# Performance work log

Hardware: AMD Instinct MI355X
Metric: run time of the kernel (lower is better)

The kernel has to match this reference:

```python
import jax, jax.numpy as jnp
from jax import lax
import numpy as np

B = 128   # per-stream batch (hard-coded via torch.zeros(128, ...))
T = 224   # timesteps
L = 224   # per-timestep signal length
H = 12    # LSTM hidden size


def _conv_chain(x, w1, b1, w2, b2):
    # x: [N, 1, 224] -> [N, 1, 28]
    # Conv1d(k=8, s=4, p=2) -> ReLU -> MaxPool1d(k=4, s=2, p=1) -> ReLU -> Conv1d(k=3, s=1, p=1) -> ReLU
    y = lax.conv_general_dilated(x, w1, (4,), [(2, 2)]) + b1[None, :, None]          # [N,1,56]
    y = jax.nn.relu(y)
    y = lax.reduce_window(y, -jnp.inf, lax.max, (1, 1, 4), (1, 1, 2),
                          [(0, 0), (0, 0), (1, 1)])                                   # [N,1,28]
    y = jax.nn.relu(y)
    y = lax.conv_general_dilated(y, w2, (1,), [(1, 1)]) + b2[None, :, None]          # [N,1,28]
    return jax.nn.relu(y)


def _lstm_bidir(x, Wih, Whh, b):
    # x: [B, T, D]; Wih: [2, 4H, D]; Whh: [2, 4H, H]; b: [2, 4H]; gates in PyTorch order i,f,g,o
    Bn, hid = x.shape[0], Whh.shape[-1]

    def run(xs, wih, whh, bb):
        def step(carry, xt):
            h, c = carry
            g = xt @ wih.T + h @ whh.T + bb
            i, f, gg, o = jnp.split(g, 4, axis=-1)
            c = jax.nn.sigmoid(f) * c + jax.nn.sigmoid(i) * jnp.tanh(gg)
            h = jax.nn.sigmoid(o) * jnp.tanh(c)
            return (h, c), h
        h0 = jnp.zeros((Bn, hid), x.dtype)
        _, ys = lax.scan(step, (h0, h0), xs)
        return ys

    xs = jnp.swapaxes(x, 0, 1)                     # [T, B, D]
    fwd = run(xs, Wih[0], Whh[0], b[0])
    bwd = run(xs[::-1], Whh_fix := Wih[1], Whh[1], b[1])[::-1]
    return jnp.swapaxes(jnp.concatenate([fwd, bwd], axis=-1), 0, 1)  # [B, T, 2H]


def _forward(x, c1w1, c1b1, c1w2, c1b2, c2w1, c2b1, c2w2, c2b2,
             l1_0_Wih, l1_0_Whh, l1_0_b, l1_1_Wih, l1_1_Whh, l1_1_b,
             l2_0_Wih, l2_0_Whh, l2_0_b, l2_1_Wih, l2_1_Whh, l2_1_b,
             fcw1, fcb1, fcw2, fcb2, fcw3, fcb3, w1, w2):
    x1 = x[:B, 0]          # [B, 224, 224]
    x2 = x[B:2 * B, 0]     # [B, 224, 224]
    # Fuse the 224-step Python loop: fold time into the batch of the 1D conv.
    y1 = _conv_chain(x1.reshape(B * T, 1, L), c1w1, c1b1, c1w2, c1b2).reshape(B, T, 28)
    y2 = _conv_chain(x2.reshape(B * T, 1, L), c2w1, c2b1, c2w2, c2b2).reshape(B, T, 28)
    o1 = _lstm_bidir(_lstm_bidir(y1, l1_0_Wih, l1_0_Whh, l1_0_b), l1_1_Wih, l1_1_Whh, l1_1_b)
    o2 = _lstm_bidir(_lstm_bidir(y2, l2_0_Wih, l2_0_Whh, l2_0_b), l2_1_Wih, l2_1_Whh, l2_1_b)
    out = w1 * o1 + w2 * o2                       # [B, T, 24]
    out = out.reshape(B, T * 2 * H)               # [B, 5376]
    out = out @ fcw1.T + fcb1                     # [B, 1024]
    out = out @ fcw2.T + fcb2                     # [B, 192]
    return out @ fcw3.T + fcb3                    # [B, 9]


def setup_inputs():
    key = jax.random.key(0)
    ks = iter(jax.random.split(key, 48))

    def rn(shape, scale=0.1):
        return (scale * jax.random.normal(next(ks), shape)).astype(jnp.float32)

    inp = {"x": rn((2 * B, 1, T, L), 1.0)}
    for s in ("c1", "c2"):
        inp[s + "w1"] = rn((1, 1, 8))
        inp[s + "b1"] = rn((1,))
        inp[s + "w2"] = rn((1, 1, 3))
        inp[s + "b2"] = rn((1,))
    for s in ("l1", "l2"):
        for layer, din in ((0, 28), (1, 2 * H)):
            inp[f"{s}_{layer}_Wih"] = rn((2, 4 * H, din))
            inp[f"{s}_{layer}_Whh"] = rn((2, 4 * H, H))
            inp[f"{s}_{layer}_b"] = rn((2, 4 * H))
    inp["fcw1"] = rn((1024, T * 2 * H), 0.02)
    inp["fcb1"] = rn((1024,))
    inp["fcw2"] = rn((192, 1024), 0.05)
    inp["fcb2"] = rn((192,))
    inp["fcw3"] = rn((9, 192), 0.05)
    inp["fcb3"] = rn((9,))
    inp["w1"] = jnp.ones((1,), jnp.float32)
    inp["w2"] = jnp.ones((1,), jnp.float32)
    return inp


def reference(x, c1w1, c1b1, c1w2, c1b2, c2w1, c2b1, c2w2, c2b2,
              l1_0_Wih, l1_0_Whh, l1_0_b, l1_1_Wih, l1_1_Whh, l1_1_b,
              l2_0_Wih, l2_0_Whh, l2_0_b, l2_1_Wih, l2_1_Whh, l2_1_b,
              fcw1, fcb1, fcw2, fcb2, fcw3, fcb3, w1, w2):
    return _forward(x, c1w1, c1b1, c1w2, c1b2, c2w1, c2b1, c2w2, c2b2,
                    l1_0_Wih, l1_0_Whh, l1_0_b, l1_1_Wih, l1_1_Whh, l1_1_b,
                    l2_0_Wih, l2_0_Whh, l2_0_b, l2_1_Wih, l2_1_Whh, l2_1_b,
                    fcw1, fcb1, fcw2, fcb2, fcw3, fcb3, w1, w2)
```

## Files before the change

kernel.cpp:

```cpp
#include <hip/hip_runtime.h>

#define BB 128
#define TT 224
#define LL 224

typedef float v2f __attribute__((ext_vector_type(2)));

__device__ __forceinline__ float rcpf(float x){ return __builtin_amdgcn_rcpf(x); }

#if __has_builtin(__builtin_amdgcn_exp2f)
#define EXP2(x) __builtin_amdgcn_exp2f(x)
#else
#define EXP2(x) __expf((x)*0.6931471805599453f)
#endif

template<int N>
__device__ __forceinline__ float rorN(float x){
  int xi = __builtin_bit_cast(int, x);
  xi = __builtin_amdgcn_update_dpp(xi, xi, 0x120 + N, 0xf, 0xf, false);
  return __builtin_bit_cast(float, xi);
}

__device__ __forceinline__ void swap32(float& a, float& b){
  asm volatile("s_nop 1\n\tv_permlane32_swap_b32 %0, %1\n\ts_nop 1"
               : "+v"(a), "+v"(b));
}

#define LSTM_STEP(P, SS) { \
  float x1=rorN<1>(hv), x2=rorN<2>(hv), x3=rorN<3>(hv), x4=rorN<4>(hv), \
        x5=rorN<5>(hv), x6=rorN<6>(hv), x7=rorN<7>(hv), x8=rorN<8>(hv), \
        x9=rorN<9>(hv), x10=rorN<10>(hv), x11=rorN<11>(hv), x12=rorN<12>(hv), \
        x13=rorN<13>(hv), x14=rorN<14>(hv), x15=rorN<15>(hv); \
  v2f a0 = (P); \
  a0 += w[0]*(v2f){hv,hv};   a0 += w[1]*(v2f){x1,x1};   a0 += w[2]*(v2f){x2,x2};   a0 += w[3]*(v2f){x3,x3}; \
  v2f a1 = w[4]*(v2f){x4,x4};   a1 += w[5]*(v2f){x5,x5};   a1 += w[6]*(v2f){x6,x6};   a1 += w[7]*(v2f){x7,x7}; \
  v2f a2 = w[8]*(v2f){x8,x8};   a2 += w[9]*(v2f){x9,x9};   a2 += w[10]*(v2f){x10,x10}; a2 += w[11]*(v2f){x11,x11}; \
  v2f a3 = w[12]*(v2f){x12,x12}; a3 += w[13]*(v2f){x13,x13}; a3 += w[14]*(v2f){x14,x14}; a3 += w[15]*(v2f){x15,x15}; \
  v2f gg = (a0+a1)+(a2+a3); \
  v2f m  = gg*kmul; \
  v2f e  = { EXP2(m.x), EXP2(m.y) }; \
  e += (v2f){1.f,1.f}; \
  v2f d  = { rcpf(e.x), rcpf(e.y) }; \
  v2f res = ca*d + cb; \
  float p0 = res.x, p1 = res.x; swap32(p0, p1); \
  float q0 = res.y, q1 = res.y; swap32(q0, q1); \
  cst = fmaf(q0, cst, p0*p1); \
  float et = EXP2(cst*2.885390082f); \
  float dt = rcpf(et+1.f); \
  hv = q1*fmaf(-2.f, dt, 1.f); \
  hbuf[SS] = hv; }

#define FLUSH8 { \
  if (doSt){ \
    _Pragma("unroll") \
    for (int q=0;q<8;q++) outP[q*ostep] = hbuf[q]; \
  } \
  outP += 8*ostep; }

#define LSTM_PREP(WHH) \
  v2f w[16]; \
  _Pragma("unroll") \
  for (int rr=0; rr<16; rr++){ \
    int j = (u - rr) & 15; \
    bool vld = (j < 12) && (u < 12); \
    int uw = (u < 12) ? u : 0; \
    int jw = (j < 12) ? j : 0; \
    float wa = (WHH)[((rbit?24:0)  + uw)*12 + jw]; \
    float wb = (WHH)[((rbit?36:12) + uw)*12 + jw]; \
    w[rr] = (v2f){ vld ? wa : 0.f, vld ? wb : 0.f }; \
  } \
  const v2f kmul = rbit ? (v2f){2.885390082f, -1.442695041f} \
                        : (v2f){-1.442695041f, -1.442695041f}; \
  const v2f ca   = rbit ? (v2f){-2.f, 1.f} : (v2f){1.f, 1.f}; \
  const v2f cb   = rbit ? (v2f){ 1.f, 0.f} : (v2f){0.f, 0.f};

#define LSTM_CONSUME_LDS(LPRE, OUTBUF) { \
  float* preR = (LPRE) + bh*(224*48) + keff*4 + rbit*2; \
  const int sstep = dir ? -48 : 48; \
  int scb = dir ? 223*48 : 0; \
  volatile int* pv = prog; \
  while (pv[1] < 2 || pv[2] < 2) __builtin_amdgcn_s_sleep(2); \
  asm volatile("" ::: "memory"); \
  v2f pcur[8], pnext[8]; \
  _Pragma("unroll") \
  for (int i=0;i<8;i++) pcur[i]  = *(const v2f*)(preR + scb +  i   *sstep); \
  _Pragma("unroll") \
  for (int i=0;i<8;i++) pnext[i] = *(const v2f*)(preR + scb + (i+8)*sstep); \
  int lb = scb + 16*sstep; \
  float hv = 0.f, cst = 0.f; \
  float hbuf[8]; \
  const int ostep = dir ? -24 : 24; \
  float* outP = (OUTBUF) + (size_t)br*(BB*TT*24) + (size_t)b*TT*24 + dir*12 + u \
              + (size_t)(dir ? 223 : 0)*24; \
  const bool doSt = (rbit==0) && (u < 12); \
  for (int c=0;c<14;c++){ \
    LSTM_STEP(pcur[0],0) LSTM_STEP(pcur[1],1) LSTM_STEP(pcur[2],2) LSTM_STEP(pcur[3],3) \
    LSTM_STEP(pcur[4],4) LSTM_STEP(pcur[5],5) LSTM_STEP(pcur[6],6) LSTM_STEP(pcur[7],7) \
    FLUSH8 \
    if (c < 13){ \
      int nd_ = 2*c+3; \
      while (pv[1] < nd_ || pv[2] < nd_) __builtin_amdgcn_s_sleep(2); \
      asm volatile("" ::: "memory"); \
      _Pragma("unroll") \
      for (int i=0;i<8;i++) pcur[i] = *(const v2f*)(preR + lb + i*sstep); \
      lb += 8*sstep; \
    } \
    LSTM_STEP(pnext[0],0) LSTM_STEP(pnext[1],1) LSTM_STEP(pnext[2],2) LSTM_STEP(pnext[3],3) \
    LSTM_STEP(pnext[4],4) LSTM_STEP(pnext[5],5) LSTM_STEP(pnext[6],6) LSTM_STEP(pnext[7],7) \
    FLUSH8 \
    if (c < 13){ \
      int nd_ = 2*c+4; \
      while (pv[1] < nd_ || pv[2] < nd_) __builtin_amdgcn_s_sleep(2); \
      asm volatile("" ::: "memory"); \
      _Pragma("unroll") \
      for (int i=0;i<8;i++) pnext[i] = *(const v2f*)(preR + lb + i*sstep); \
      lb += 8*sstep; \
    } \
  } }

__global__ __launch_bounds__(256) void fcA_kernel(
    const float* __restrict__ fcw1, const float* __restrict__ fcw2,
    const float* __restrict__ fcw3, const float* __restrict__ fcb1,
    float* __restrict__ wpart, float* __restrict__ BCpart)
{
  __shared__ float sb[2880];
  int gb  = blockIdx.x;
  int tid = threadIdx.x;
  int s     = gb / 21;
  int jtile = gb % 21;
  float* wtp = sb;
  float* wt  = sb + 2304;
  {
    int wave = tid >> 6, lane = tid & 63;
    float acc[9];
    #pragma unroll
    for (int q=0;q<9;q++) acc[q]=0.f;
    const float* f2 = fcw2 + s*64 + lane;
    int p0 = wave*48;
    #pragma unroll 4
    for (int pp=0; pp<48; pp++){
      int p = p0 + pp;
      float v = f2[(size_t)p*1024];
      #pragma unroll
      for (int q=0;q<9;q++) acc[q] += fcw3[q*192+p]*v;
    }
    #pragma unroll
    for (int q=0;q<9;q++) wtp[wave*576 + q*64 + lane] = acc[q];
  }
  __syncthreads();
  for (int i = tid; i < 576; i += 256)
    wt[i] = wtp[i] + wtp[576+i] + wtp[1152+i] + wtp[1728+i];
  __syncthreads();

  int j = jtile*256 + tid;
  int nbase = s*64;
  float acc[9];
  #pragma unroll
  for (int o=0;o<9;o++) acc[o]=0.f;
  #pragma unroll 4
  for (int n4=0;n4<16;n4++){
    int nb = nbase + n4*4;
    float4 v4;
    v4.x = fcw1[(size_t)(nb  )*5376 + j];
    v4.y = fcw1[(size_t)(nb+1)*5376 + j];
    v4.z = fcw1[(size_t)(nb+2)*5376 + j];
    v4.w = fcw1[(size_t)(nb+3)*5376 + j];
    #pragma unroll
    for (int o=0;o<9;o++){
      float4 w4 = *(const float4*)&wt[o*64 + n4*4];
      acc[o] += v4.x*w4.x + v4.y*w4.y + v4.z*w4.z + v4.w*w4.w;
    }
  }
  #pragma unroll
  for (int o=0;o<9;o++) wpart[((size_t)s*9+o)*5376 + j] = acc[o];
  if (jtile == 0 && tid < 9){
    float bcp = 0.f;
    for (int n=0;n<64;n++) bcp += wt[tid*64+n]*fcb1[nbase+n];
    BCpart[s*9+tid] = bcp;
  }
}

__global__ __launch_bounds__(256) __attribute__((amdgpu_waves_per_eu(1,1)))
void lstm1_fused_kernel(const float* __restrict__ x,
    const float* __restrict__ whhA, const float* __restrict__ whhB,
    const float* __restrict__ wihA, const float* __restrict__ biasA,
    const float* __restrict__ wihB, const float* __restrict__ biasB,
    const float* __restrict__ c1w1, const float* __restrict__ c1b1,
    const float* __restrict__ c1w2, const float* __restrict__ c1b2,
    const float* __restrict__ c2w1, const float* __restrict__ c2b1,
    const float* __restrict__ c2w2, const float* __restrict__ c2b2,
    float* __restrict__ out)
{
  __shared__ float lpre[2*224*48];
  __shared__ float ybuf[2*224*28];
  __shared__ float c1s[16*57];
  __shared__ int prog[8];
  int tid  = threadIdx.x;
  int blk  = blockIdx.x;
  int r    = blk >> 6;
  int br   = r >> 1, dir = r & 1;
  int b0   = (blk & 63)*2;

  if (tid < 8) ((volatile int*)prog)[tid] = 0;
  __syncthreads();

  if (tid >= 64 && tid < 128){
    int p    = tid - 64;
    int rowq = p >> 2;
    int q    = p & 3;
    int bb   = rowq >> 3;
    int ti   = rowq & 7;
    int cjs  = q*14;
    const float* w1 = br ? c2w1 : c1w1;
    const float* w2 = br ? c2w2 : c1w2;
    float b1  = br ? c2b1[0] : c1b1[0];
    float b2v = br ? c2b2[0] : c1b2[0];
    float w1r[8];
    #pragma unroll
    for (int kk=0;kk<8;kk++) w1r[kk]=w1[kk];
    float w2r[3];
    #pragma unroll
    for (int kk=0;kk<3;kk++) w2r[kk]=w2[kk];
    const float* xb = x + ((size_t)(br*128 + b0 + bb))*50176;
    volatile int* pv = prog;
    int a0 = 4*cjs - 4;

    for (int g=0; g<28; ++g){
      int step = g*8 + ti;
      int t = dir ? 223-step : step;
      const float* xrow = xb + (size_t)t*224;
      float xr[64];
      #pragma unroll
      for (int qq=0; qq<16; qq++){
        int idx = a0 + 4*qq;
        if (idx >= 0 && idx <= 220){
          float4 v = *(const float4*)(xrow + idx);
          xr[4*qq]=v.x; xr[4*qq+1]=v.y; xr[4*qq+2]=v.z; xr[4*qq+3]=v.w;
        } else {
          #pragma unroll
          for (int e=0;e<4;e++){
            int ii = idx+e;
            xr[4*qq+e] = (ii>=0 && ii<224) ? xrow[ii] : 0.f;
          }
        }
      }
      #pragma unroll
      for (int e=0;e<14;e++){
        float s = b1;
        #pragma unroll
        for (int kk=0;kk<8;kk++) s += xr[4*e+2+kk]*w1r[kk];
        c1s[rowq*57 + cjs + e] = fmaxf(s, 0.f);
      }
      asm volatile("s_waitcnt lgkmcnt(0)" ::: "memory");
      const float* cr = &c1s[rowq*57];
      #pragma unroll
      for (int jj=0;jj<7;jj++){
        int j = q*7 + jj;
        float o = b2v;
        #pragma unroll
        for (int pi=0;pi<3;pi++){
          int pp = j - 1 + pi;
          float pool = 0.f;
          if (pp>=0 && pp<28){
            int i0 = 2*pp - 1;
            float m = -1e30f;
            #pragma unroll
            for (int q2=0;q2<4;q2++){
              int ii = i0+q2;
              if (ii>=0 && ii<56) m = fmaxf(m, cr[ii]);
            }
            pool = fmaxf(m, 0.f);
          }
          o += pool * w2r[pi];
        }
        ybuf[(bb*224 + t)*28 + j] = fmaxf(o, 0.f);
      }
      asm volatile("s_waitcnt lgkmcnt(0)" ::: "memory");
      if (p == 0) pv[0] = g+1;
    }
    return;
  }

  if (tid >= 128){
    int p2 = tid - 128;
    if (p2 >= 96) return;
    int fidx = (tid >> 6) - 1;
    int bb   = p2 / 48;
    int gate = p2 % 48;
    const float* wih2 = (br ? wihB : wihA) + (dir*48 + gate)*28;
    float4 wq[7];
    #pragma unroll
    for (int q=0;q<7;q++) wq[q] = ((const float4*)wih2)[q];
    float bias = (br ? biasB : biasA)[dir*48 + gate];
    int unit = gate % 12, gg = gate / 12;
    float* lrow = lpre + bb*(224*48) + unit*4 + gg;
    volatile int* pv = prog;

    for (int g=0; g<28; ++g){
      while (pv[0] < g+1) __builtin_amdgcn_s_sleep(2);
      asm volatile("" ::: "memory");
      #pragma unroll
      for (int si=0; si<8; si++){
        int t = dir ? 223-(g*8+si) : (g*8+si);
        const float4* yr = (const float4*)&ybuf[(bb*224 + t)*28];
        float a = bias;
        #pragma unroll
        for (int q=0;q<7;q++){
          float4 yq = yr[q];
          a += yq.x*wq[q].x + yq.y*wq[q].y + yq.z*wq[q].z + yq.w*wq[q].w;
        }
        lrow[t*48] = a;
      }
      asm volatile("s_waitcnt lgkmcnt(0)" ::: "memory");
      if ((p2 & 63) == 0) pv[fidx] = g+1;
    }
    return;
  }

  int lane = tid;
  int u    = lane & 15;
  int bh   = (lane >> 4) & 1;
  int rbit = lane >> 5;
  int keff = (u < 12) ? u : 11;
  int b    = b0 + bh;
  const float* whh = (br ? whhB : whhA) + dir*48*12;
  LSTM_PREP(whh)
  LSTM_CONSUME_LDS(lpre, out)
}

__global__ __launch_bounds__(256) __attribute__((amdgpu_waves_per_eu(1,1)))
void lstm2_fused_kernel(const float* __restrict__ ol0,
    const float* __restrict__ whhA, const float* __restrict__ whhB,
    const float* __restrict__ wihA, const float* __restrict__ biasA,
    const float* __restrict__ wihB, const float* __restrict__ biasB,
    float* __restrict__ out)
{
  __shared__ float lpre[2*224*48];
  __shared__ int prog[8];
  int tid  = threadIdx.x;
  int blk  = blockIdx.x;
  int r    = blk >> 6;
  int br   = r >> 1, dir = r & 1;
  int b0   = (blk & 63)*2;

  if (tid < 8) ((volatile int*)prog)[tid] = 0;
  __syncthreads();

  if (tid >= 64){
    int p    = tid - 64;
    int wv   = p >> 6;
    int e    = p % 96;
    int th   = p / 96;
    int bb   = e / 48;
    int gate = e % 48;
    const float* wih2 = (br ? wihB : wihA) + (dir*48 + gate)*24;
    float4 wq[6];
    #pragma unroll
    for (int q=0;q<6;q++) wq[q] = ((const float4*)wih2)[q];
    float bias = (br ? biasB : biasA)[dir*48 + gate];
    int unit = gate % 12, gg = gate / 12;
    const float* olrow = ol0 + (size_t)br*(BB*TT*24) + (size_t)(b0+bb)*TT*24;
    float* lrow = lpre + bb*(224*48) + unit*4 + gg;
    volatile int* pv = prog;

    for (int g=0; g<28; g++){
      #pragma unroll
      for (int si=0; si<4; si++){
        int step = g*8 + th*4 + si;
        int t = dir ? 223 - step : step;
        const float4* xr = (const float4*)(olrow + t*24);
        float a = bias;
        #pragma unroll
        for (int q=0;q<6;q++){
          float4 xq = xr[q];
          a += xq.x*wq[q].x + xq.y*wq[q].y + xq.z*wq[q].z + xq.w*wq[q].w;
        }
        lrow[t*48] = a;
      }
      asm volatile("s_waitcnt lgkmcnt(0) vmcnt(0)" ::: "memory");
      if ((p & 63) == 0) pv[wv] = g+1;
    }
    return;
  }

  int lane = tid;
  int u    = lane & 15;
  int bh   = (lane >> 4) & 1;
  int rbit = lane >> 5;
  int keff = (u < 12) ? u : 11;
  int b    = b0 + bh;
  const float* whh = (br ? whhB : whhA) + dir*48*12;
  LSTM_PREP(whh)
  {
    float* preR = lpre + bh*(224*48) + keff*4 + rbit*2;
    const int sstep = dir ? -48 : 48;
    int scb = dir ? 223*48 : 0;
    volatile int* pv = prog;
#define WAITG3(NEED) { int nd_ = (NEED); \
  while (pv[0] < nd_ || pv[1] < nd_ || pv[2] < nd_) __builtin_amdgcn_s_sleep(2); \
  asm volatile("" ::: "memory"); }
    WAITG3(2)
    v2f pcur[8], pnext[8];
    #pragma unroll
    for (int i=0;i<8;i++) pcur[i]  = *(const v2f*)(preR + scb +  i   *sstep);
    #pragma unroll
    for (int i=0;i<8;i++) pnext[i] = *(const v2f*)(preR + scb + (i+8)*sstep);
    int lb = scb + 16*sstep;
    float hv = 0.f, cst = 0.f;
    float hbuf[8];
    const int ostep = dir ? -24 : 24;
    float* outP = out + (size_t)br*(BB*TT*24) + (size_t)b*TT*24 + dir*12 + u
                + (size_t)(dir ? 223 : 0)*24;
    const bool doSt = (rbit==0) && (u < 12);
    for (int c=0;c<14;c++){
      LSTM_STEP(pcur[0],0) LSTM_STEP(pcur[1],1) LSTM_STEP(pcur[2],2) LSTM_STEP(pcur[3],3)
      LSTM_STEP(pcur[4],4) LSTM_STEP(pcur[5],5) LSTM_STEP(pcur[6],6) LSTM_STEP(pcur[7],7)
      FLUSH8
      if (c < 13){
        WAITG3(2*c+3)
        #pragma unroll
        for (int i=0;i<8;i++) pcur[i] = *(const v2f*)(preR + lb + i*sstep);
        lb += 8*sstep;
      }
      LSTM_STEP(pnext[0],0) LSTM_STEP(pnext[1],1) LSTM_STEP(pnext[2],2) LSTM_STEP(pnext[3],3)
      LSTM_STEP(pnext[4],4) LSTM_STEP(pnext[5],5) LSTM_STEP(pnext[6],6) LSTM_STEP(pnext[7],7)
      FLUSH8
      if (c < 13){
        WAITG3(2*c+4)
        #pragma unroll
        for (int i=0;i<8;i++) pnext[i] = *(const v2f*)(preR + lb + i*sstep);
        lb += 8*sstep;
      }
    }
#undef WAITG3
  }
}

__global__ __launch_bounds__(256) void wpartB_kernel(
    const float* __restrict__ wpart, float* __restrict__ Wc,
    const float* __restrict__ fcw3, const float* __restrict__ fcb2,
    const float* __restrict__ fcb3, const float* __restrict__ BCpart,
    float* __restrict__ BC)
{
  int gb  = blockIdx.x;
  int tid = threadIdx.x;
  if (gb < 189){
    int idx = gb*256 + tid;
    float a = 0.f;
    #pragma unroll
    for (int s=0;s<16;s++) a += wpart[(size_t)s*48384 + idx];
    Wc[idx] = a;
  } else if (tid < 9){
    float acc = fcb3[tid];
    const float* f3 = fcw3 + tid*192;
    for (int p=0;p<192;p++) acc += f3[p]*fcb2[p];
    #pragma unroll
    for (int s=0;s<16;s++) acc += BCpart[s*9+tid];
    BC[tid] = acc;
  }
}

__global__ void final_kernel(const float* __restrict__ o1, const float* __restrict__ o2,
    const float* __restrict__ Wc, const float* __restrict__ BC,
    const float* __restrict__ w1p, const float* __restrict__ w2p,
    float* __restrict__ out)
{
  int wid  = blockIdx.x*4 + (threadIdx.x>>6);
  int lane = threadIdx.x & 63;
  if (wid >= 128*9) return;
  int m = wid / 9, o = wid - m*9;
  float w1 = w1p[0], w2 = w2p[0];
  const float* r1 = o1 + (size_t)m*5376;
  const float* r2 = o2 + (size_t)m*5376;
  const float* wc = Wc + (size_t)o*5376;
  float acc = 0.f;
  for (int i=lane;i<5376;i+=64){
    acc += (w1*r1[i] + w2*r2[i]) * wc[i];
  }
  #pragma unroll
  for (int off=32;off;off>>=1) acc += __shfl_down(acc, off);
  if (lane==0) out[m*9+o] = acc + BC[o];
}

extern "C" void kernel_launch(void* const* d_in, const int* in_sizes, int n_in,
                              void* d_out, int out_size, void* d_ws, size_t ws_size,
                              hipStream_t stream) {
  (void)in_sizes; (void)n_in; (void)out_size; (void)ws_size;
  const float* x    = (const float*)d_in[0];
  const float* c1w1 = (const float*)d_in[1];
  const float* c1b1 = (const float*)d_in[2];
  const float* c1w2 = (const float*)d_in[3];
  const float* c1b2 = (const float*)d_in[4];
  const float* c2w1 = (const float*)d_in[5];
  const float* c2b1 = (const float*)d_in[6];
  const float* c2w2 = (const float*)d_in[7];
  const float* c2b2 = (const float*)d_in[8];
  const float* l10Wih = (const float*)d_in[9];
  const float* l10Whh = (const float*)d_in[10];
  const float* l10b   = (const float*)d_in[11];
  const float* l11Wih = (const float*)d_in[12];
  const float* l11Whh = (const float*)d_in[13];
  const float* l11b   = (const float*)d_in[14];
  const float* l20Wih = (const float*)d_in[15];
  const float* l20Whh = (const float*)d_in[16];
  const float* l20b   = (const float*)d_in[17];
  const float* l21Wih = (const float*)d_in[18];
  const float* l21Whh = (const float*)d_in[19];
  const float* l21b   = (const float*)d_in[20];
  const float* fcw1 = (const float*)d_in[21];
  const float* fcb1 = (const float*)d_in[22];
  const float* fcw2 = (const float*)d_in[23];
  const float* fcb2 = (const float*)d_in[24];
  const float* fcw3 = (const float*)d_in[25];
  const float* fcb3 = (const float*)d_in[26];
  const float* w1   = (const float*)d_in[27];
  const float* w2   = (const float*)d_in[28];
  float* out = (float*)d_out;

  float* ws  = (float*)d_ws;
  float* wpart = ws;
  float* ol0  = ws + 2*802816 + 4*1376256;
  float* ol1  = ol0 + 2*688128;
  float* Wc   = ol1 + 2*688128;
  float* BC   = Wc  + 48384;
  float* BCpart = BC + 9;

  fcA_kernel<<<336,256,0,stream>>>(fcw1, fcw2, fcw3, fcb1, wpart, BCpart);
  lstm1_fused_kernel<<<256,256,0,stream>>>(x, l10Whh, l20Whh,
      l10Wih, l10b, l20Wih, l20b,
      c1w1,c1b1,c1w2,c1b2, c2w1,c2b1,c2w2,c2b2, ol0);
  wpartB_kernel<<<190,256,0,stream>>>(wpart, Wc, fcw3, fcb2, fcb3, BCpart, BC);
  lstm2_fused_kernel<<<256,256,0,stream>>>(ol0, l11Whh, l21Whh,
      l11Wih, l11b, l21Wih, l21b, ol1);
  final_kernel<<<288,256,0,stream>>>(ol1, ol1+688128, Wc, BC, w1, w2, out);
}
```

Measured before the change: 159.3 us.

## Fold FC weight precomputation into idle producer waves of the LSTM kernels

Removes the standalone fcA and wpartB kernels. A small wtb kernel now precomputes fcw3·fcw2. Producer waves in lstm1 run the fcw1 folding after their conv and projection work, and producer waves in lstm2 do the wpart reduction and bias combination. The aim is to hide these weight-only matmuls behind the latency-bound LSTM recurrences and to cut two launches. The risk is that the extra global traffic on the producer waves delays the recurrence waves if those waves are not fully idle, and the lstm1 consumers now also wait on pv[0].

```diff
diff --git a/kernel.cpp b/kernel.cpp
--- a/kernel.cpp
+++ b/kernel.cpp
@@ -74,12 +74,12 @@
   const v2f ca   = rbit ? (v2f){-2.f, 1.f} : (v2f){1.f, 1.f}; \
   const v2f cb   = rbit ? (v2f){ 1.f, 0.f} : (v2f){0.f, 0.f};
 
-#define LSTM_CONSUME_LDS(LPRE, OUTBUF) { \
+#define LSTM_CONSUME3(LPRE, OUTBUF) { \
   float* preR = (LPRE) + bh*(224*48) + keff*4 + rbit*2; \
   const int sstep = dir ? -48 : 48; \
   int scb = dir ? 223*48 : 0; \
   volatile int* pv = prog; \
-  while (pv[1] < 2 || pv[2] < 2) __builtin_amdgcn_s_sleep(2); \
+  while (pv[0] < 2 || pv[1] < 2 || pv[2] < 2) __builtin_amdgcn_s_sleep(2); \
   asm volatile("" ::: "memory"); \
   v2f pcur[8], pnext[8]; \
   _Pragma("unroll") \
@@ -99,7 +99,7 @@
     FLUSH8 \
     if (c < 13){ \
       int nd_ = 2*c+3; \
-      while (pv[1] < nd_ || pv[2] < nd_) __builtin_amdgcn_s_sleep(2); \
+      while (pv[0] < nd_ || pv[1] < nd_ || pv[2] < nd_) __builtin_amdgcn_s_sleep(2); \
       asm volatile("" ::: "memory"); \
       _Pragma("unroll") \
       for (int i=0;i<8;i++) pcur[i] = *(const v2f*)(preR + lb + i*sstep); \
@@ -110,7 +110,7 @@
     FLUSH8 \
     if (c < 13){ \
       int nd_ = 2*c+4; \
-      while (pv[1] < nd_ || pv[2] < nd_) __builtin_amdgcn_s_sleep(2); \
+      while (pv[0] < nd_ || pv[1] < nd_ || pv[2] < nd_) __builtin_amdgcn_s_sleep(2); \
       asm volatile("" ::: "memory"); \
       _Pragma("unroll") \
       for (int i=0;i<8;i++) pnext[i] = *(const v2f*)(preR + lb + i*sstep); \
@@ -118,66 +118,15 @@
     } \
   } }
 
-__global__ __launch_bounds__(256) void fcA_kernel(
-    const float* __restrict__ fcw1, const float* __restrict__ fcw2,
-    const float* __restrict__ fcw3, const float* __restrict__ fcb1,
-    float* __restrict__ wpart, float* __restrict__ BCpart)
+__global__ __launch_bounds__(256) void wtb_kernel(
+    const float* __restrict__ fcw2, const float* __restrict__ fcw3,
+    float* __restrict__ Wtb)
 {
-  __shared__ float sb[2880];
-  int gb  = blockIdx.x;
-  int tid = threadIdx.x;
-  int s     = gb / 21;
-  int jtile = gb % 21;
-  float* wtp = sb;
-  float* wt  = sb + 2304;
-  {
-    int wave = tid >> 6, lane = tid & 63;
-    float acc[9];
-    #pragma unroll
-    for (int q=0;q<9;q++) acc[q]=0.f;
-    const float* f2 = fcw2 + s*64 + lane;
-    int p0 = wave*48;
-    #pragma unroll 4
-    for (int pp=0; pp<48; pp++){
-      int p = p0 + pp;
-      float v = f2[(size_t)p*1024];
-      #pragma unroll
-      for (int q=0;q<9;q++) acc[q] += fcw3[q*192+p]*v;
-    }
-    #pragma unroll
-    for (int q=0;q<9;q++) wtp[wave*576 + q*64 + lane] = acc[q];
-  }
-  __syncthreads();
-  for (int i = tid; i < 576; i += 256)
-    wt[i] = wtp[i] + wtp[576+i] + wtp[1152+i] + wtp[1728+i];
-  __syncthreads();
-
-  int j = jtile*256 + tid;
-  int nbase = s*64;
-  float acc[9];
-  #pragma unroll
-  for (int o=0;o<9;o++) acc[o]=0.f;
-  #pragma unroll 4
-  for (int n4=0;n4<16;n4++){
-    int nb = nbase + n4*4;
-    float4 v4;
-    v4.x = fcw1[(size_t)(nb  )*5376 + j];
-    v4.y = fcw1[(size_t)(nb+1)*5376 + j];
-    v4.z = fcw1[(size_t)(nb+2)*5376 + j];
-    v4.w = fcw1[(size_t)(nb+3)*5376 + j];
-    #pragma unroll
-    for (int o=0;o<9;o++){
-      float4 w4 = *(const float4*)&wt[o*64 + n4*4];
-      acc[o] += v4.x*w4.x + v4.y*w4.y + v4.z*w4.z + v4.w*w4.w;
-    }
-  }
-  #pragma unroll
-  for (int o=0;o<9;o++) wpart[((size_t)s*9+o)*5376 + j] = acc[o];
-  if (jtile == 0 && tid < 9){
-    float bcp = 0.f;
-    for (int n=0;n<64;n++) bcp += wt[tid*64+n]*fcb1[nbase+n];
-    BCpart[s*9+tid] = bcp;
-  }
+  int idx = blockIdx.x*256 + threadIdx.x;
+  int o = idx >> 10, n = idx & 1023;
+  float acc = 0.f;
+  for (int p=0;p<192;p++) acc += fcw3[o*192+p]*fcw2[(size_t)p*1024+n];
+  Wtb[idx] = acc;
 }
 
 __global__ __launch_bounds__(256) __attribute__((amdgpu_waves_per_eu(1,1)))
@@ -189,11 +138,15 @@
     const float* __restrict__ c1w2, const float* __restrict__ c1b2,
     const float* __restrict__ c2w1, const float* __restrict__ c2b1,
     const float* __restrict__ c2w2, const float* __restrict__ c2b2,
+    const float* __restrict__ fcw1, const float* __restrict__ fcb1,
+    const float* __restrict__ Wtb,
+    float* __restrict__ wpart, float* __restrict__ BCpart,
     float* __restrict__ out)
 {
   __shared__ float lpre[2*224*48];
   __shared__ float ybuf[2*224*28];
   __shared__ float c1s[16*57];
+  __shared__ float wtscr[3*576];
   __shared__ int prog[8];
   int tid  = threadIdx.x;
   int blk  = blockIdx.x;
@@ -204,115 +157,154 @@
   if (tid < 8) ((volatile int*)prog)[tid] = 0;
   __syncthreads();
 
-  if (tid >= 64 && tid < 128){
-    int p    = tid - 64;
-    int rowq = p >> 2;
-    int q    = p & 3;
-    int bb   = rowq >> 3;
-    int ti   = rowq & 7;
-    int cjs  = q*14;
-    const float* w1 = br ? c2w1 : c1w1;
-    const float* w2 = br ? c2w2 : c1w2;
-    float b1  = br ? c2b1[0] : c1b1[0];
-    float b2v = br ? c2b2[0] : c1b2[0];
-    float w1r[8];
-    #pragma unroll
-    for (int kk=0;kk<8;kk++) w1r[kk]=w1[kk];
-    float w2r[3];
-    #pragma unroll
-    for (int kk=0;kk<3;kk++) w2r[kk]=w2[kk];
-    const float* xb = x + ((size_t)(br*128 + b0 + bb))*50176;
-    volatile int* pv = prog;
-    int a0 = 4*cjs - 4;
-
-    for (int g=0; g<28; ++g){
-      int step = g*8 + ti;
-      int t = dir ? 223-step : step;
-      const float* xrow = xb + (size_t)t*224;
-      float xr[64];
+  if (tid >= 64){
+    if (tid < 128){
+      int p    = tid - 64;
+      int rowq = p >> 2;
+      int q    = p & 3;
+      int bb   = rowq >> 3;
+      int ti   = rowq & 7;
+      int cjs  = q*14;
+      const float* w1 = br ? c2w1 : c1w1;
+      const float* w2 = br ? c2w2 : c1w2;
+      float b1  = br ? c2b1[0] : c1b1[0];
+      float b2v = br ? c2b2[0] : c1b2[0];
+      float w1r[8];
       #pragma unroll
-      for (int qq=0; qq<16; qq++){
-        int idx = a0 + 4*qq;
-        if (idx >= 0 && idx <= 220){
-          float4 v = *(const float4*)(xrow + idx);
-          xr[4*qq]=v.x; xr[4*qq+1]=v.y; xr[4*qq+2]=v.z; xr[4*qq+3]=v.w;
-        } else {
+      for (int kk=0;kk<8;kk++) w1r[kk]=w1[kk];
+      float w2r[3];
+      #pragma unroll
+      for (int kk=0;kk<3;kk++) w2r[kk]=w2[kk];
+      const float* xb = x + ((size_t)(br*128 + b0 + bb))*50176;
+      volatile int* pv = prog;
+      int a0 = 4*cjs - 4;
+
+      for (int g=0; g<28; ++g){
+        int step = g*8 + ti;
+        int t = dir ? 223-step : step;
+        const float* xrow = xb + (size_t)t*224;
+        float xr[64];
+        #pragma unroll
+        for (int qq=0; qq<16; qq++){
+          int idx = a0 + 4*qq;
+          if (idx >= 0 && idx <= 220){
+            float4 v = *(const float4*)(xrow + idx);
+            xr[4*qq]=v.x; xr[4*qq+1]=v.y; xr[4*qq+2]=v.z; xr[4*qq+3]=v.w;
+          } else {
+            #pragma unroll
+            for (int e=0;e<4;e++){
+              int ii = idx+e;
+              xr[4*qq+e] = (ii>=0 && ii<224) ? xrow[ii] : 0.f;
+            }
+          }
+        }
+        #pragma unroll
+        for (int e=0;e<14;e++){
+          float s = b1;
           #pragma unroll
-          for (int e=0;e<4;e++){
-            int ii = idx+e;
-            xr[4*qq+e] = (ii>=0 && ii<224) ? xrow[ii] : 0.f;
+          for (int kk=0;kk<8;kk++) s += xr[4*e+2+kk]*w1r[kk];
+          c1s[rowq*57 + cjs + e] = fmaxf(s, 0.f);
+        }
+        asm volatile("s_waitcnt lgkmcnt(0)" ::: "memory");
+        const float* cr = &c1s[rowq*57];
+        #pragma unroll
+        for (int jj=0;jj<7;jj++){
+          int j = q*7 + jj;
+          float o = b2v;
+          #pragma unroll
+          for (int pi=0;pi<3;pi++){
+            int pp = j - 1 + pi;
+            float pool = 0.f;
+            if (pp>=0 && pp<28){
+              int i0 = 2*pp - 1;
+              float m = -1e30f;
+              #pragma unroll
+              for (int q2=0;q2<4;q2++){
+                int ii = i0+q2;
+                if (ii>=0 && ii<56) m = fmaxf(m, cr[ii]);
+              }
+              pool = fmaxf(m, 0.f);
+            }
+            o += pool * w2r[pi];
           }
-        }
-      }
-      #pragma unroll
-      for (int e=0;e<14;e++){
-        float s = b1;
-        #pragma unroll
-        for (int kk=0;kk<8;kk++) s += xr[4*e+2+kk]*w1r[kk];
-        c1s[rowq*57 + cjs + e] = fmaxf(s, 0.f);
-      }
-      asm volatile("s_waitcnt lgkmcnt(0)" ::: "memory");
-      const float* cr = &c1s[rowq*57];
-      #pragma unroll
-      for (int jj=0;jj<7;jj++){
-        int j = q*7 + jj;
-        float o = b2v;
-        #pragma unroll
-        for (int pi=0;pi<3;pi++){
-          int pp = j - 1 + pi;
-          float pool = 0.f;
-          if (pp>=0 && pp<28){
-            int i0 = 2*pp - 1;
-            float m = -1e30f;
+          ybuf[(bb*224 + t)*28 + j] = fmaxf(o, 0.f);
+        }
+        asm volatile("s_waitcnt lgkmcnt(0)" ::: "memory");
+        if (p == 0) pv[0] = g+1;
+      }
+    } else {
+      int p2 = tid - 128;
+      if (p2 < 96){
+        int fidx = (tid >> 6) - 1;
+        int bb   = p2 / 48;
+        int gate = p2 % 48;
+        const float* wih2 = (br ? wihB : wihA) + (dir*48 + gate)*28;
+        float4 wq[7];
+        #pragma unroll
+        for (int q=0;q<7;q++) wq[q] = ((const float4*)wih2)[q];
+        float bias = (br ? biasB : biasA)[dir*48 + gate];
+        int unit = gate % 12, gg = gate / 12;
+        float* lrow = lpre + bb*(224*48) + unit*4 + gg;
+        volatile int* pv = prog;
+
+        for (int g=0; g<28; ++g){
+          while (pv[0] < g+1) __builtin_amdgcn_s_sleep(2);
+          asm volatile("" ::: "memory");
+          #pragma unroll
+          for (int si=0; si<8; si++){
+            int t = dir ? 223-(g*8+si) : (g*8+si);
+            const float4* yr = (const float4*)&ybuf[(bb*224 + t)*28];
+            float a = bias;
             #pragma unroll
-            for (int q2=0;q2<4;q2++){
-              int ii = i0+q2;
-              if (ii>=0 && ii<56) m = fmaxf(m, cr[ii]);
+            for (int q=0;q<7;q++){
+              float4 yq = yr[q];
+              a += yq.x*wq[q].x + yq.y*wq[q].y + yq.z*wq[q].z + yq.w*wq[q].w;
             }
-            pool = fmaxf(m, 0.f);
+            lrow[t*48] = a;
           }
-          o += pool * w2r[pi];
-        }
-        ybuf[(bb*224 + t)*28 + j] = fmaxf(o, 0.f);
-      }
-      asm volatile("s_waitcnt lgkmcnt(0)" ::: "memory");
-      if (p == 0) pv[0] = g+1;
+          asm volatile("s_waitcnt lgkmcnt(0)" ::: "memory");
+          if ((p2 & 63) == 0) pv[fidx] = g+1;
+        }
+      }
     }
-    return;
-  }
-
-  if (tid >= 128){
-    int p2 = tid - 128;
-    if (p2 >= 96) return;
-    int fidx = (tid >> 6) - 1;
-    int bb   = p2 / 48;
-    int gate = p2 % 48;
-    const float* wih2 = (br ? wihB : wihA) + (dir*48 + gate)*28;
-    float4 wq[7];
-    #pragma unroll
-    for (int q=0;q<7;q++) wq[q] = ((const float4*)wih2)[q];
-    float bias = (br ? biasB : biasA)[dir*48 + gate];
-    int unit = gate % 12, gg = gate / 12;
-    float* lrow = lpre + bb*(224*48) + unit*4 + gg;
-    volatile int* pv = prog;
-
-    for (int g=0; g<28; ++g){
-      while (pv[0] < g+1) __builtin_amdgcn_s_sleep(2);
-      asm volatile("" ::: "memory");
-      #pragma unroll
-      for (int si=0; si<8; si++){
-        int t = dir ? 223-(g*8+si) : (g*8+si);
-        const float4* yr = (const float4*)&ybuf[(bb*224 + t)*28];
-        float a = bias;
-        #pragma unroll
-        for (int q=0;q<7;q++){
-          float4 yq = yr[q];
-          a += yq.x*wq[q].x + yq.y*wq[q].y + yq.z*wq[q].z + yq.w*wq[q].w;
-        }
-        lrow[t*48] = a;
-      }
-      asm volatile("s_waitcnt lgkmcnt(0)" ::: "memory");
-      if ((p2 & 63) == 0) pv[fidx] = g+1;
+
+    {
+      int wv   = (tid >> 6) - 1;
+      int lane = tid & 63;
+      float* wt = wtscr + wv*576;
+      for (int tk = blk*3 + wv; tk < 1344; tk += 768){
+        int s = tk / 84, j64 = tk % 84;
+        #pragma unroll
+        for (int q=0;q<9;q++) wt[q*64+lane] = Wtb[q*1024 + s*64 + lane];
+        asm volatile("s_waitcnt lgkmcnt(0) vmcnt(0)" ::: "memory");
+        int j = j64*64 + lane;
+        int nbase = s*64;
+        float acc[9];
+        #pragma unroll
+        for (int o=0;o<9;o++) acc[o]=0.f;
+        #pragma unroll 4
+        for (int n4=0;n4<16;n4++){
+          int nb = nbase + n4*4;
+          float4 v4;
+          v4.x = fcw1[(size_t)(nb  )*5376 + j];
+          v4.y = fcw1[(size_t)(nb+1)*5376 + j];
+          v4.z = fcw1[(size_t)(nb+2)*5376 + j];
+          v4.w = fcw1[(size_t)(nb+3)*5376 + j];
+          #pragma unroll
+          for (int o=0;o<9;o++){
+            float4 w4 = *(const float4*)&wt[o*64 + n4*4];
+            acc[o] += v4.x*w4.x + v4.y*w4.y + v4.z*w4.z + v4.w*w4.w;
+          }
+        }
+        #pragma unroll
+        for (int o=0;o<9;o++) wpart[((size_t)s*9+o)*5376 + j] = acc[o];
+        if (j64 == 0 && lane < 9){
+          float bcp = 0.f;
+          for (int n=0;n<64;n++) bcp += wt[lane*64+n]*fcb1[nbase+n];
+          BCpart[s*9+lane] = bcp;
+        }
+        asm volatile("s_waitcnt lgkmcnt(0)" ::: "memory");
+      }
     }
     return;
   }
@@ -325,7 +317,7 @@
   int b    = b0 + bh;
   const float* whh = (br ? whhB : whhA) + dir*48*12;
   LSTM_PREP(whh)
-  LSTM_CONSUME_LDS(lpre, out)
+  LSTM_CONSUME3(lpre, out)
 }
 
 __global__ __launch_bounds__(256) __attribute__((amdgpu_waves_per_eu(1,1)))
@@ -333,6 +325,10 @@
     const float* __restrict__ whhA, const float* __restrict__ whhB,
     const float* __restrict__ wihA, const float* __restrict__ biasA,
     const float* __restrict__ wihB, const float* __restrict__ biasB,
+    const float* __restrict__ wpart, float* __restrict__ Wc,
+    const float* __restrict__ fcw3, const float* __restrict__ fcb2,
+    const float* __restrict__ fcb3, const float* __restrict__ BCpart,
+    float* __restrict__ BC,
     float* __restrict__ out)
 {
   __shared__ float lpre[2*224*48];
@@ -380,6 +376,26 @@
       asm volatile("s_waitcnt lgkmcnt(0) vmcnt(0)" ::: "memory");
       if ((p & 63) == 0) pv[wv] = g+1;
     }
+
+    {
+      int lane = p & 63;
+      int tk = blk*3 + wv;
+      if (tk < 756){
+        int idx = tk*64 + lane;
+        float a = 0.f;
+        #pragma unroll
+        for (int s=0;s<16;s++) a += wpart[(size_t)s*48384 + idx];
+        Wc[idx] = a;
+      }
+      if (blk == 255 && wv == 2 && lane < 9){
+        float acc = fcb3[lane];
+        const float* f3 = fcw3 + lane*192;
+        for (int pp=0;pp<192;pp++) acc += f3[pp]*fcb2[pp];
+        #pragma unroll
+        for (int s=0;s<16;s++) acc += BCpart[s*9+lane];
+        BC[lane] = acc;
+      }
+    }
     return;
   }
 
@@ -391,73 +407,7 @@
   int b    = b0 + bh;
   const float* whh = (br ? whhB : whhA) + dir*48*12;
   LSTM_PREP(whh)
-  {
-    float* preR = lpre + bh*(224*48) + keff*4 + rbit*2;
-    const int sstep = dir ? -48 : 48;
-    int scb = dir ? 223*48 : 0;
-    volatile int* pv = prog;
-#define WAITG3(NEED) { int nd_ = (NEED); \
-  while (pv[0] < nd_ || pv[1] < nd_ || pv[2] < nd_) __builtin_amdgcn_s_sleep(2); \
-  asm volatile("" ::: "memory"); }
-    WAITG3(2)
-    v2f pcur[8], pnext[8];
-    #pragma unroll
-    for (int i=0;i<8;i++) pcur[i]  = *(const v2f*)(preR + scb +  i   *sstep);
-    #pragma unroll
-    for (int i=0;i<8;i++) pnext[i] = *(const v2f*)(preR + scb + (i+8)*sstep);
-    int lb = scb + 16*sstep;
-    float hv = 0.f, cst = 0.f;
-    float hbuf[8];
-    const int ostep = dir ? -24 : 24;
-    float* outP = out + (size_t)br*(BB*TT*24) + (size_t)b*TT*24 + dir*12 + u
-                + (size_t)(dir ? 223 : 0)*24;
-    const bool doSt = (rbit==0) && (u < 12);
-    for (int c=0;c<14;c++){
-      LSTM_STEP(pcur[0],0) LSTM_STEP(pcur[1],1) LSTM_STEP(pcur[2],2) LSTM_STEP(pcur[3],3)
-      LSTM_STEP(pcur[4],4) LSTM_STEP(pcur[5],5) LSTM_STEP(pcur[6],6) LSTM_STEP(pcur[7],7)
-      FLUSH8
-      if (c < 13){
-        WAITG3(2*c+3)
-        #pragma unroll
-        for (int i=0;i<8;i++) pcur[i] = *(const v2f*)(preR + lb + i*sstep);
-        lb += 8*sstep;
-      }
-      LSTM_STEP(pnext[0],0) LSTM_STEP(pnext[1],1) LSTM_STEP(pnext[2],2) LSTM_STEP(pnext[3],3)
-      LSTM_STEP(pnext[4],4) LSTM_STEP(pnext[5],5) LSTM_STEP(pnext[6],6) LSTM_STEP(pnext[7],7)
-      FLUSH8
-      if (c < 13){
-        WAITG3(2*c+4)
-        #pragma unroll
-        for (int i=0;i<8;i++) pnext[i] = *(const v2f*)(preR + lb + i*sstep);
-        lb += 8*sstep;
-      }
-    }
-#undef WAITG3
-  }
-}
-
-__global__ __launch_bounds__(256) void wpartB_kernel(
-    const float* __restrict__ wpart, float* __restrict__ Wc,
-    const float* __restrict__ fcw3, const float* __restrict__ fcb2,
-    const float* __restrict__ fcb3, const float* __restrict__ BCpart,
-    float* __restrict__ BC)
-{
-  int gb  = blockIdx.x;
-  int tid = threadIdx.x;
-  if (gb < 189){
-    int idx = gb*256 + tid;
-    float a = 0.f;
-    #pragma unroll
-    for (int s=0;s<16;s++) a += wpart[(size_t)s*48384 + idx];
-    Wc[idx] = a;
-  } else if (tid < 9){
-    float acc = fcb3[tid];
-    const float* f3 = fcw3 + tid*192;
-    for (int p=0;p<192;p++) acc += f3[p]*fcb2[p];
-    #pragma unroll
-    for (int s=0;s<16;s++) acc += BCpart[s*9+tid];
-    BC[tid] = acc;
-  }
+  LSTM_CONSUME3(lpre, out)
 }
 
 __global__ void final_kernel(const float* __restrict__ o1, const float* __restrict__ o2,
@@ -524,13 +474,15 @@
   float* Wc   = ol1 + 2*688128;
   float* BC   = Wc  + 48384;
   float* BCpart = BC + 9;
-
-  fcA_kernel<<<336,256,0,stream>>>(fcw1, fcw2, fcw3, fcb1, wpart, BCpart);
+  float* Wtb  = BCpart + 144;
+
+  wtb_kernel<<<36,256,0,stream>>>(fcw2, fcw3, Wtb);
   lstm1_fused_kernel<<<256,256,0,stream>>>(x, l10Whh, l20Whh,
       l10Wih, l10b, l20Wih, l20b,
-      c1w1,c1b1,c1w2,c1b2, c2w1,c2b1,c2w2,c2b2, ol0);
-  wpartB_kernel<<<190,256,0,stream>>>(wpart, Wc, fcw3, fcb2, fcb3, BCpart, BC);
+      c1w1,c1b1,c1w2,c1b2, c2w1,c2b1,c2w2,c2b2,
+      fcw1, fcb1, Wtb, wpart, BCpart, ol0);
   lstm2_fused_kernel<<<256,256,0,stream>>>(ol0, l11Whh, l21Whh,
-      l11Wih, l11b, l21Wih, l21b, ol1);
+      l11Wih, l11b, l21Wih, l21b,
+      wpart, Wc, fcw3, fcb2, fcb3, BCpart, BC, ol1);
   final_kernel<<<288,256,0,stream>>>(ol1, ol1+688128, Wc, BC, w1, w2, out);
 }
```

After: 152.4 us, median of 3. -4.3%, faster.
